# Kernel optimization log

Measured on AMD Instinct MI355X. Metric: run time of the kernel, lower is better.

Reference implementation:

```python
import jax, jax.numpy as jnp
import numpy as np

N, E, D_IN, D_OUT = 50000, 800000, 96, 256
BN_EPS = 1e-3  # Keras BatchNormalization default epsilon


def setup_inputs() -> dict:
    key = jax.random.key(0)
    ks = jax.random.split(key, 8)
    return {
        "x": jax.random.normal(ks[0], (N, D_IN), dtype=jnp.float32),
        "adj_src": jax.random.randint(ks[1], (E,), 0, N, dtype=jnp.int32),
        "adj_dst": jax.random.randint(ks[2], (E,), 0, N, dtype=jnp.int32),
        "adj_vals": jax.random.uniform(ks[3], (E,), dtype=jnp.float32),
        "eps": jax.random.normal(ks[4], (1,), dtype=jnp.float32) * 0.05,
        "W0": jax.random.normal(ks[5], (D_IN, D_OUT), dtype=jnp.float32) * 0.05,
        "W1": jax.random.normal(ks[6], (D_OUT, D_OUT), dtype=jnp.float32) * 0.05,
        "gamma": jnp.ones((D_OUT,), dtype=jnp.float32),
        "beta": jnp.zeros((D_OUT,), dtype=jnp.float32),
        "bn_mean": jnp.zeros((D_OUT,), dtype=jnp.float32),
        "bn_var": jnp.ones((D_OUT,), dtype=jnp.float32),
    }


def reference(x, adj_src, adj_dst, adj_vals, eps, W0, W1, gamma, beta, bn_mean, bn_var):
    n = x.shape[0]
    # Sparse adjacency SpMM: out[d] = sum_{e: dst(e)=d} vals[e] * x[src(e)]
    msgs = adj_vals[:, None] * x[adj_src]              # [E, D_IN]
    agg = jax.ops.segment_sum(msgs, adj_dst, num_segments=n)  # [N, D_IN]
    h = agg + eps * x                                   # eps residual (GIN)
    # MLP layer 0: matmul -> BN (inference) -> ReLU (dropout identity at eval)
    h = h @ W0                                           # [N, D_OUT]
    h = (h - bn_mean) * jax.lax.rsqrt(bn_var + BN_EPS) * gamma + beta
    h = jax.nn.relu(h)
    # Final matmul
    return h @ W1                                        # [N, D_OUT]
```

## Files before the change

### kernel.cpp

```cpp
#include <hip/hip_runtime.h>

#define D_IN   96
#define D_OUT  256
#define BN_EPS 1e-3f
#define TROWS  32
#define CAP    64
#define N_PAD  50048
#define RS1    104
#define RS2    264

typedef __attribute__((ext_vector_type(8))) short  short8;
typedef __attribute__((ext_vector_type(4))) float  floatx4;

__device__ __forceinline__ unsigned short f2bf(float f) {
    unsigned int u = __float_as_uint(f);
    unsigned int r = u + 0x7FFFu + ((u >> 16) & 1u);
    return (unsigned short)(r >> 16);
}
__device__ __forceinline__ float bfbits(unsigned short u) {
    return __uint_as_float(((unsigned int)u) << 16);
}

#define SCAT(S, D, V) do {                                                  \
    unsigned int u_ = __float_as_uint(V);                                   \
    unsigned int vhi_ = (u_ + 0x7FFFu + ((u_ >> 16) & 1u)) & 0xFFFF0000u;   \
    int pos_ = atomicAdd(&cursor[(D)], 1);                                  \
    if (pos_ < CAP)                                                         \
        bucket[((D) << 6) + pos_] = (int)(vhi_ | (unsigned int)(S));        \
} while (0)

__global__ __launch_bounds__(256) void prep(
    const int* __restrict__ src, const int* __restrict__ dst,
    const float* __restrict__ vals, const float* __restrict__ x,
    const float* __restrict__ W0, const float* __restrict__ W1,
    int* __restrict__ cursor, int* __restrict__ bucket,
    unsigned short* __restrict__ xbf,
    unsigned short* __restrict__ W0p, unsigned short* __restrict__ W1p,
    int E, int n, int nscat, int nxc)
{
    const int b = blockIdx.x, tid = threadIdx.x;
    if (b < nscat) {
        int t = (b * 256 + tid) * 4;
        if (t + 4 <= E) {
            int4   s4 = *(const int4*)  (src  + t);
            int4   d4 = *(const int4*)  (dst  + t);
            float4 v4 = *(const float4*)(vals + t);
            SCAT(s4.x, d4.x, v4.x);
            SCAT(s4.y, d4.y, v4.y);
            SCAT(s4.z, d4.z, v4.z);
            SCAT(s4.w, d4.w, v4.w);
        } else if (t < E) {
            for (int q = t; q < E; ++q) {
                int S = src[q], D = dst[q]; float V = vals[q];
                SCAT(S, D, V);
            }
        }
    } else if (b < nscat + nxc) {
        size_t t   = (size_t)(b - nscat) * 256 + tid;
        size_t off = t * 8;
        if (off < (size_t)n * D_IN) {
            float4 v0 = *(const float4*)(x + off);
            float4 v1 = *(const float4*)(x + off + 4);
            ushort4 o0, o1;
            o0.x = f2bf(v0.x); o0.y = f2bf(v0.y); o0.z = f2bf(v0.z); o0.w = f2bf(v0.w);
            o1.x = f2bf(v1.x); o1.y = f2bf(v1.y); o1.z = f2bf(v1.z); o1.w = f2bf(v1.w);
            *(ushort4*)(xbf + off)     = o0;
            *(ushort4*)(xbf + off + 4) = o1;
        }
    } else {
        int o = (b - nscat - nxc) * 256 + tid;
        const int n0 = 3 * 256 * 32;
        const int n1 = 8 * 256 * 32;
        if (o < n0) {
            int kk = o & 31, nn = (o >> 5) & 255, kb = o >> 13;
            W0p[o] = f2bf(W0[(size_t)(kb * 32 + kk) * 256 + nn]);
        } else if (o < n0 + n1) {
            int o2 = o - n0;
            int kk = o2 & 31, nn = (o2 >> 5) & 255, kb = o2 >> 13;
            W1p[o2] = f2bf(W1[(size_t)(kb * 32 + kk) * 256 + nn]);
        }
    }
}
#undef SCAT

template<bool BF16X>
__global__ __launch_bounds__(256, 8) void gin_fused(
    const float* __restrict__ x, const unsigned short* __restrict__ xbf,
    const int* __restrict__ deg, const int* __restrict__ bucket,
    const float* __restrict__ epsp,
    const unsigned short* __restrict__ W0p, const unsigned short* __restrict__ W1p,
    const float* __restrict__ gamma, const float* __restrict__ beta,
    const float* __restrict__ bn_mean, const float* __restrict__ bn_var,
    float* __restrict__ out, int n)
{
    __shared__ __align__(16) unsigned short SMEM[TROWS * RS2];
    __shared__ float bn_scale[D_OUT];
    __shared__ float bn_shift[D_OUT];
    unsigned short (*Abuf)[RS1] = (unsigned short (*)[RS1])SMEM;
    unsigned short (*Hbuf)[RS2] = (unsigned short (*)[RS2])SMEM;

    const int tid = threadIdx.x;
    const int rowbase = blockIdx.x * TROWS;
    const float epsv = *epsp;

    {
        float sc = gamma[tid] * rsqrtf(bn_var[tid] + BN_EPS);
        bn_scale[tid] = sc;
        bn_shift[tid] = fmaf(-bn_mean[tid], sc, beta[tid]);
    }

    {
        const int j   = tid & 7;
        const int rl  = tid >> 3;
        const int row = rowbase + rl;
        float acc[12];
#pragma unroll
        for (int q = 0; q < 12; ++q) acc[q] = 0.f;

        if (row < n) {
            const int dg = min(deg[row], CAP);
            const int* ep = bucket + (row << 6);

#define EDGE_FMA(vv, A, B, C)                                              \
            { acc[0] = fmaf(vv, A.x, acc[0]); acc[1] = fmaf(vv, A.y, acc[1]);  \
              acc[2] = fmaf(vv, A.z, acc[2]); acc[3] = fmaf(vv, A.w, acc[3]);  \
              acc[4] = fmaf(vv, B.x, acc[4]); acc[5] = fmaf(vv, B.y, acc[5]);  \
              acc[6] = fmaf(vv, B.z, acc[6]); acc[7] = fmaf(vv, B.w, acc[7]);  \
              acc[8] = fmaf(vv, C.x, acc[8]); acc[9] = fmaf(vv, C.y, acc[9]);  \
              acc[10] = fmaf(vv, C.z, acc[10]); acc[11] = fmaf(vv, C.w, acc[11]); }

            int e = 0;
            if (BF16X) {
                const unsigned short* rr = xbf + (size_t)row * D_IN + j * 12;
                ushort4 sa = *(const ushort4*)(rr);
                ushort4 sb = *(const ushort4*)(rr + 4);
                ushort4 sc = *(const ushort4*)(rr + 8);

                for (; e + 2 <= dg; e += 2) {
                    int p0 = __builtin_nontemporal_load(ep + e);
                    int p1 = __builtin_nontemporal_load(ep + e + 1);
                    float v0 = __uint_as_float((unsigned int)p0 & 0xFFFF0000u);
                    float v1 = __uint_as_float((unsigned int)p1 & 0xFFFF0000u);
                    const unsigned short* r0 = xbf + (size_t)(p0 & 0xFFFF) * D_IN + j * 12;
                    const unsigned short* r1 = xbf + (size_t)(p1 & 0xFFFF) * D_IN + j * 12;
                    ushort4 a0 = *(const ushort4*)(r0), b0 = *(const ushort4*)(r0 + 4), c0 = *(const ushort4*)(r0 + 8);
                    ushort4 a1 = *(const ushort4*)(r1), b1 = *(const ushort4*)(r1 + 4), c1 = *(const ushort4*)(r1 + 8);
                    float4 A, B, C;
                    A.x = bfbits(a0.x); A.y = bfbits(a0.y); A.z = bfbits(a0.z); A.w = bfbits(a0.w);
                    B.x = bfbits(b0.x); B.y = bfbits(b0.y); B.z = bfbits(b0.z); B.w = bfbits(b0.w);
                    C.x = bfbits(c0.x); C.y = bfbits(c0.y); C.z = bfbits(c0.z); C.w = bfbits(c0.w);
                    EDGE_FMA(v0, A, B, C)
                    A.x = bfbits(a1.x); A.y = bfbits(a1.y); A.z = bfbits(a1.z); A.w = bfbits(a1.w);
                    B.x = bfbits(b1.x); B.y = bfbits(b1.y); B.z = bfbits(b1.z); B.w = bfbits(b1.w);
                    C.x = bfbits(c1.x); C.y = bfbits(c1.y); C.z = bfbits(c1.z); C.w = bfbits(c1.w);
                    EDGE_FMA(v1, A, B, C)
                }
                for (; e < dg; ++e) {
                    int p0 = __builtin_nontemporal_load(ep + e);
                    float v0 = __uint_as_float((unsigned int)p0 & 0xFFFF0000u);
                    const unsigned short* r0 = xbf + (size_t)(p0 & 0xFFFF) * D_IN + j * 12;
                    ushort4 a0 = *(const ushort4*)(r0), b0 = *(const ushort4*)(r0 + 4), c0 = *(const ushort4*)(r0 + 8);
                    float4 A, B, C;
                    A.x = bfbits(a0.x); A.y = bfbits(a0.y); A.z = bfbits(a0.z); A.w = bfbits(a0.w);
                    B.x = bfbits(b0.x); B.y = bfbits(b0.y); B.z = bfbits(b0.z); B.w = bfbits(b0.w);
                    C.x = bfbits(c0.x); C.y = bfbits(c0.y); C.z = bfbits(c0.z); C.w = bfbits(c0.w);
                    EDGE_FMA(v0, A, B, C)
                }
                {
                    float4 A, B, C;
                    A.x = bfbits(sa.x); A.y = bfbits(sa.y); A.z = bfbits(sa.z); A.w = bfbits(sa.w);
                    B.x = bfbits(sb.x); B.y = bfbits(sb.y); B.z = bfbits(sb.z); B.w = bfbits(sb.w);
                    C.x = bfbits(sc.x); C.y = bfbits(sc.y); C.z = bfbits(sc.z); C.w = bfbits(sc.w);
                    EDGE_FMA(epsv, A, B, C)
                }
            } else {
                for (; e + 2 <= dg; e += 2) {
                    int p0 = __builtin_nontemporal_load(ep + e);
                    int p1 = __builtin_nontemporal_load(ep + e + 1);
                    float v0 = __uint_as_float((unsigned int)p0 & 0xFFFF0000u);
                    float v1 = __uint_as_float((unsigned int)p1 & 0xFFFF0000u);
                    const float* r0 = x + (size_t)(p0 & 0xFFFF) * D_IN + j * 12;
                    const float* r1 = x + (size_t)(p1 & 0xFFFF) * D_IN + j * 12;
                    float4 A0 = *(const float4*)(r0), B0 = *(const float4*)(r0 + 4), C0 = *(const float4*)(r0 + 8);
                    float4 A1 = *(const float4*)(r1), B1 = *(const float4*)(r1 + 4), C1 = *(const float4*)(r1 + 8);
                    EDGE_FMA(v0, A0, B0, C0)
                    EDGE_FMA(v1, A1, B1, C1)
                }
                for (; e < dg; ++e) {
                    int p0 = __builtin_nontemporal_load(ep + e);
                    float v0 = __uint_as_float((unsigned int)p0 & 0xFFFF0000u);
                    const float* r0 = x + (size_t)(p0 & 0xFFFF) * D_IN + j * 12;
                    float4 A0 = *(const float4*)(r0), B0 = *(const float4*)(r0 + 4), C0 = *(const float4*)(r0 + 8);
                    EDGE_FMA(v0, A0, B0, C0)
                }
                const float* rr = x + (size_t)row * D_IN + j * 12;
                float4 A0 = *(const float4*)(rr), B0 = *(const float4*)(rr + 4), C0 = *(const float4*)(rr + 8);
                EDGE_FMA(epsv, A0, B0, C0)
            }
#undef EDGE_FMA
        }
#pragma unroll
        for (int q = 0; q < 6; ++q) {
            unsigned int lo = f2bf(acc[2 * q]);
            unsigned int hi = f2bf(acc[2 * q + 1]);
            *(unsigned int*)&Abuf[rl][j * 12 + 2 * q] = lo | (hi << 16);
        }
    }
    __syncthreads();

    const int lane = tid & 63;
    const int wid  = tid >> 6;
    const int quad = lane >> 4;
    const int nl   = lane & 15;

    floatx4 acc1[2][4];
#pragma unroll
    for (int mt = 0; mt < 2; ++mt)
#pragma unroll
        for (int nt = 0; nt < 4; ++nt)
            acc1[mt][nt] = (floatx4){0.f, 0.f, 0.f, 0.f};

#pragma unroll
    for (int kb = 0; kb < 3; ++kb) {
        short8 af0 = *(const short8*)&Abuf[nl     ][kb * 32 + quad * 8];
        short8 af1 = *(const short8*)&Abuf[16 + nl][kb * 32 + quad * 8];
#pragma unroll
        for (int nt = 0; nt < 4; ++nt) {
            const unsigned short* bp =
                W0p + ((size_t)(kb * 256 + wid * 64 + nt * 16 + nl)) * 32 + quad * 8;
            short8 bf = *(const short8*)bp;
            acc1[0][nt] = __builtin_amdgcn_mfma_f32_16x16x32_bf16(af0, bf, acc1[0][nt], 0, 0, 0);
            acc1[1][nt] = __builtin_amdgcn_mfma_f32_16x16x32_bf16(af1, bf, acc1[1][nt], 0, 0, 0);
        }
    }
    __syncthreads();

#pragma unroll
    for (int mt = 0; mt < 2; ++mt)
#pragma unroll
        for (int nt = 0; nt < 4; ++nt) {
            int ncol = wid * 64 + nt * 16 + nl;
            float sc = bn_scale[ncol], sh = bn_shift[ncol];
#pragma unroll
            for (int r = 0; r < 4; ++r) {
                float h = fmaxf(0.f, fmaf(acc1[mt][nt][r], sc, sh));
                Hbuf[mt * 16 + quad * 4 + r][ncol] = f2bf(h);
            }
        }
    __syncthreads();

    floatx4 acc2[2][4];
#pragma unroll
    for (int mt = 0; mt < 2; ++mt)
#pragma unroll
        for (int nt = 0; nt < 4; ++nt)
            acc2[mt][nt] = (floatx4){0.f, 0.f, 0.f, 0.f};

#pragma unroll
    for (int kb = 0; kb < 8; ++kb) {
        short8 af0 = *(const short8*)&Hbuf[nl     ][kb * 32 + quad * 8];
        short8 af1 = *(const short8*)&Hbuf[16 + nl][kb * 32 + quad * 8];
#pragma unroll
        for (int nt = 0; nt < 4; ++nt) {
            const unsigned short* bp =
                W1p + ((size_t)(kb * 256 + wid * 64 + nt * 16 + nl)) * 32 + quad * 8;
            short8 bf = *(const short8*)bp;
            acc2[0][nt] = __builtin_amdgcn_mfma_f32_16x16x32_bf16(af0, bf, acc2[0][nt], 0, 0, 0);
            acc2[1][nt] = __builtin_amdgcn_mfma_f32_16x16x32_bf16(af1, bf, acc2[1][nt], 0, 0, 0);
        }
    }

#pragma unroll
    for (int mt = 0; mt < 2; ++mt)
#pragma unroll
        for (int nt = 0; nt < 4; ++nt) {
            int ncol = wid * 64 + nt * 16 + nl;
#pragma unroll
            for (int r = 0; r < 4; ++r) {
                int m = rowbase + mt * 16 + quad * 4 + r;
                if (m < n)
                    __builtin_nontemporal_store(acc2[mt][nt][r],
                                                out + (size_t)m * D_OUT + ncol);
            }
        }
}

extern "C" void kernel_launch(void* const* d_in, const int* in_sizes, int n_in,
                              void* d_out, int out_size, void* d_ws, size_t ws_size,
                              hipStream_t stream) {
    const float* x       = (const float*)d_in[0];
    const int*   src     = (const int*)  d_in[1];
    const int*   dst     = (const int*)  d_in[2];
    const float* vals    = (const float*)d_in[3];
    const float* epsp    = (const float*)d_in[4];
    const float* W0      = (const float*)d_in[5];
    const float* W1      = (const float*)d_in[6];
    const float* gamma   = (const float*)d_in[7];
    const float* beta    = (const float*)d_in[8];
    const float* bn_mean = (const float*)d_in[9];
    const float* bn_var  = (const float*)d_in[10];
    float* out = (float*)d_out;

    const int n = in_sizes[0] / D_IN;
    const int E = in_sizes[1];

    int* cursor = (int*)d_ws;
    int* bucket = cursor + N_PAD;
    unsigned short* W0p = (unsigned short*)(bucket + (size_t)n * CAP);
    unsigned short* W1p = W0p + 3 * 256 * 32;
    unsigned short* xbf = W1p + 8 * 256 * 32;

    const size_t base_need = (size_t)(N_PAD + (size_t)n * CAP) * 4
                           + (size_t)(3 + 8) * 256 * 32 * 2;
    const bool use_bf16x = ws_size >= base_need + (size_t)n * D_IN * 2;

    hipMemsetAsync(cursor, 0, (size_t)n * sizeof(int), stream);

    const int nscat = (E + 1023) / 1024;
    const int nxc   = use_bf16x ? ((n * D_IN / 8) + 255) / 256 : 0;
    const int nwc   = ((3 + 8) * 256 * 32 + 255) / 256;
    prep<<<nscat + nxc + nwc, 256, 0, stream>>>(
        src, dst, vals, x, W0, W1, cursor, bucket, xbf, W0p, W1p, E, n, nscat, nxc);

    const int gblocks = (n + TROWS - 1) / TROWS;
    if (use_bf16x)
        gin_fused<true><<<gblocks, 256, 0, stream>>>(
            x, xbf, cursor, bucket, epsp, W0p, W1p,
            gamma, beta, bn_mean, bn_var, out, n);
    else
        gin_fused<false><<<gblocks, 256, 0, stream>>>(
            x, xbf, cursor, bucket, epsp, W0p, W1p,
            gamma, beta, bn_mean, bn_var, out, n);
}
```

Measured before the change: 225.6 us.

## Batch-load edge bucket entries and unroll gather; one edge per thread in scatter

The gather loop now loads the first 32 bucket entries of each row as eight 16-byte vector loads and unrolls the feature-row gathers four at a time, with masked weights and clamped indices, so more independent loads are in flight. The scatter in prep now handles one edge per thread with a nontemporal store into the bucket. The occupancy hint on the fused kernel is also dropped. The trade-off is that rows with few edges still issue every bucket load, wasted masked gathers run inside the final partial group, and register pressure rises.

```diff
diff --git a/kernel.cpp b/kernel.cpp
--- a/kernel.cpp
+++ b/kernel.cpp
@@ -11,6 +11,7 @@
 
 typedef __attribute__((ext_vector_type(8))) short  short8;
 typedef __attribute__((ext_vector_type(4))) float  floatx4;
+typedef __attribute__((ext_vector_type(4))) int    intx4;
 
 __device__ __forceinline__ unsigned short f2bf(float f) {
     unsigned int u = __float_as_uint(f);
@@ -20,14 +21,6 @@
 __device__ __forceinline__ float bfbits(unsigned short u) {
     return __uint_as_float(((unsigned int)u) << 16);
 }
-
-#define SCAT(S, D, V) do {                                                  \
-    unsigned int u_ = __float_as_uint(V);                                   \
-    unsigned int vhi_ = (u_ + 0x7FFFu + ((u_ >> 16) & 1u)) & 0xFFFF0000u;   \
-    int pos_ = atomicAdd(&cursor[(D)], 1);                                  \
-    if (pos_ < CAP)                                                         \
-        bucket[((D) << 6) + pos_] = (int)(vhi_ | (unsigned int)(S));        \
-} while (0)
 
 __global__ __launch_bounds__(256) void prep(
     const int* __restrict__ src, const int* __restrict__ dst,
@@ -40,20 +33,16 @@
 {
     const int b = blockIdx.x, tid = threadIdx.x;
     if (b < nscat) {
-        int t = (b * 256 + tid) * 4;
-        if (t + 4 <= E) {
-            int4   s4 = *(const int4*)  (src  + t);
-            int4   d4 = *(const int4*)  (dst  + t);
-            float4 v4 = *(const float4*)(vals + t);
-            SCAT(s4.x, d4.x, v4.x);
-            SCAT(s4.y, d4.y, v4.y);
-            SCAT(s4.z, d4.z, v4.z);
-            SCAT(s4.w, d4.w, v4.w);
-        } else if (t < E) {
-            for (int q = t; q < E; ++q) {
-                int S = src[q], D = dst[q]; float V = vals[q];
-                SCAT(S, D, V);
-            }
+        int t = b * 256 + tid;
+        if (t < E) {
+            int d = dst[t];
+            unsigned int u = __float_as_uint(vals[t]);
+            unsigned int vhi = (u + 0x7FFFu + ((u >> 16) & 1u)) & 0xFFFF0000u;
+            int pos = atomicAdd(&cursor[d], 1);
+            if (pos < CAP)
+                __builtin_nontemporal_store(
+                    (int)(vhi | (unsigned int)src[t]),
+                    bucket + ((size_t)d << 6) + pos);
         }
     } else if (b < nscat + nxc) {
         size_t t   = (size_t)(b - nscat) * 256 + tid;
@@ -81,10 +70,9 @@
         }
     }
 }
-#undef SCAT
 
 template<bool BF16X>
-__global__ __launch_bounds__(256, 8) void gin_fused(
+__global__ __launch_bounds__(256) void gin_fused(
     const float* __restrict__ x, const unsigned short* __restrict__ xbf,
     const int* __restrict__ deg, const int* __restrict__ bucket,
     const float* __restrict__ epsp,
@@ -119,7 +107,7 @@
 
         if (row < n) {
             const int dg = min(deg[row], CAP);
-            const int* ep = bucket + (row << 6);
+            const int* ep = bucket + ((size_t)row << 6);
 
 #define EDGE_FMA(vv, A, B, C)                                              \
             { acc[0] = fmaf(vv, A.x, acc[0]); acc[1] = fmaf(vv, A.y, acc[1]);  \
@@ -129,33 +117,48 @@
               acc[8] = fmaf(vv, C.x, acc[8]); acc[9] = fmaf(vv, C.y, acc[9]);  \
               acc[10] = fmaf(vv, C.z, acc[10]); acc[11] = fmaf(vv, C.w, acc[11]); }
 
-            int e = 0;
             if (BF16X) {
+                const int nm1 = n - 1;
                 const unsigned short* rr = xbf + (size_t)row * D_IN + j * 12;
                 ushort4 sa = *(const ushort4*)(rr);
                 ushort4 sb = *(const ushort4*)(rr + 4);
                 ushort4 sc = *(const ushort4*)(rr + 8);
 
-                for (; e + 2 <= dg; e += 2) {
-                    int p0 = __builtin_nontemporal_load(ep + e);
-                    int p1 = __builtin_nontemporal_load(ep + e + 1);
-                    float v0 = __uint_as_float((unsigned int)p0 & 0xFFFF0000u);
-                    float v1 = __uint_as_float((unsigned int)p1 & 0xFFFF0000u);
-                    const unsigned short* r0 = xbf + (size_t)(p0 & 0xFFFF) * D_IN + j * 12;
-                    const unsigned short* r1 = xbf + (size_t)(p1 & 0xFFFF) * D_IN + j * 12;
-                    ushort4 a0 = *(const ushort4*)(r0), b0 = *(const ushort4*)(r0 + 4), c0 = *(const ushort4*)(r0 + 8);
-                    ushort4 a1 = *(const ushort4*)(r1), b1 = *(const ushort4*)(r1 + 4), c1 = *(const ushort4*)(r1 + 8);
-                    float4 A, B, C;
-                    A.x = bfbits(a0.x); A.y = bfbits(a0.y); A.z = bfbits(a0.z); A.w = bfbits(a0.w);
-                    B.x = bfbits(b0.x); B.y = bfbits(b0.y); B.z = bfbits(b0.z); B.w = bfbits(b0.w);
-                    C.x = bfbits(c0.x); C.y = bfbits(c0.y); C.z = bfbits(c0.z); C.w = bfbits(c0.w);
-                    EDGE_FMA(v0, A, B, C)
-                    A.x = bfbits(a1.x); A.y = bfbits(a1.y); A.z = bfbits(a1.z); A.w = bfbits(a1.w);
-                    B.x = bfbits(b1.x); B.y = bfbits(b1.y); B.z = bfbits(b1.z); B.w = bfbits(b1.w);
-                    C.x = bfbits(c1.x); C.y = bfbits(c1.y); C.z = bfbits(c1.z); C.w = bfbits(c1.w);
-                    EDGE_FMA(v1, A, B, C)
-                }
-                for (; e < dg; ++e) {
+                int w[32];
+                {
+                    const intx4* ep4 = (const intx4*)ep;
+#pragma unroll
+                    for (int q = 0; q < 8; ++q) {
+                        intx4 t = __builtin_nontemporal_load(ep4 + q);
+                        w[4 * q + 0] = t.x; w[4 * q + 1] = t.y;
+                        w[4 * q + 2] = t.z; w[4 * q + 3] = t.w;
+                    }
+                }
+
+#pragma unroll
+                for (int eb = 0; eb < 8; ++eb) {
+                    if (eb * 4 >= dg) break;
+#pragma unroll
+                    for (int u = 0; u < 4; ++u) {
+                        const int e = eb * 4 + u;
+                        int p = w[e];
+                        float v = (e < dg)
+                            ? __uint_as_float((unsigned int)p & 0xFFFF0000u)
+                            : 0.f;
+                        int idx = min(p & 0xFFFF, nm1);
+                        const unsigned short* r0 =
+                            xbf + (size_t)idx * D_IN + j * 12;
+                        ushort4 a0 = *(const ushort4*)(r0);
+                        ushort4 b0 = *(const ushort4*)(r0 + 4);
+                        ushort4 c0 = *(const ushort4*)(r0 + 8);
+                        float4 A, B, C;
+                        A.x = bfbits(a0.x); A.y = bfbits(a0.y); A.z = bfbits(a0.z); A.w = bfbits(a0.w);
+                        B.x = bfbits(b0.x); B.y = bfbits(b0.y); B.z = bfbits(b0.z); B.w = bfbits(b0.w);
+                        C.x = bfbits(c0.x); C.y = bfbits(c0.y); C.z = bfbits(c0.z); C.w = bfbits(c0.w);
+                        EDGE_FMA(v, A, B, C)
+                    }
+                }
+                for (int e = 32; e < dg; ++e) {
                     int p0 = __builtin_nontemporal_load(ep + e);
                     float v0 = __uint_as_float((unsigned int)p0 & 0xFFFF0000u);
                     const unsigned short* r0 = xbf + (size_t)(p0 & 0xFFFF) * D_IN + j * 12;
@@ -174,6 +177,7 @@
                     EDGE_FMA(epsv, A, B, C)
                 }
             } else {
+                int e = 0;
                 for (; e + 2 <= dg; e += 2) {
                     int p0 = __builtin_nontemporal_load(ep + e);
                     int p1 = __builtin_nontemporal_load(ep + e + 1);
@@ -314,9 +318,9 @@
                            + (size_t)(3 + 8) * 256 * 32 * 2;
     const bool use_bf16x = ws_size >= base_need + (size_t)n * D_IN * 2;
 
-    hipMemsetAsync(cursor, 0, (size_t)n * sizeof(int), stream);
-
-    const int nscat = (E + 1023) / 1024;
+    (void)hipMemsetAsync(cursor, 0, (size_t)n * sizeof(int), stream);
+
+    const int nscat = (E + 255) / 256;
     const int nxc   = use_bf16x ? ((n * D_IN / 8) + 255) / 256 : 0;
     const int nwc   = ((3 + 8) * 256 * 32 + 255) / 256;
     prep<<<nscat + nxc + nwc, 256, 0, stream>>>(
```

Result: faster. 199.2 us (-11.7%).
